# Optimization experiments

Hardware: AMD Instinct MI355X
Metric: run time of the kernel (lower is better)

## Reference

```python
import jax, jax.numpy as jnp
import numpy as np

N, E, H, D_IN, L, G, T = 50000, 800000, 64, 64, 4, 128, 1

def _w(key, shape, fan_in):
    return jax.random.normal(key, shape, dtype=jnp.float32) / np.sqrt(fan_in)

def setup_inputs() -> dict:
    key = jax.random.key(0)
    ks = jax.random.split(key, 24)
    inp = {
        'x': jax.random.normal(ks[0], (N, D_IN), dtype=jnp.float32),
        'w': jax.random.normal(ks[1], (E, 1), dtype=jnp.float32),
        'src': jax.random.randint(ks[2], (E,), 0, N, dtype=jnp.int32),
        'dst': jax.random.randint(ks[3], (E,), 0, N, dtype=jnp.int32),
        'graph_id': jnp.sort(jax.random.randint(ks[4], (N,), 0, G, dtype=jnp.int32)),
        # input MLP (1 layer, last_activation None; SiLU applied in input_node_func)
        'W_in': _w(ks[5], (D_IN, H), D_IN), 'b_in': jnp.zeros((H,), jnp.float32),
        # per-layer message MLP: (2H+1 -> H -> H), SiLU mid and last
        'msg_W1': _w(ks[6], (L, 2 * H + 1, H), 2 * H + 1), 'msg_b1': jnp.zeros((L, H), jnp.float32),
        'msg_W2': _w(ks[7], (L, H, H), H), 'msg_b2': jnp.zeros((L, H), jnp.float32),
        # per-layer update MLP: (H -> H -> H), SiLU mid, last None
        'upd_W1': _w(ks[8], (L, H, H), H), 'upd_b1': jnp.zeros((L, H), jnp.float32),
        'upd_W2': _w(ks[9], (L, H, H), H), 'upd_b2': jnp.zeros((L, H), jnp.float32),
        # node-wise output MLP: (H -> H -> H), SiLU mid, last None
        'out_W1': _w(ks[10], (H, H), H), 'out_b1': jnp.zeros((H,), jnp.float32),
        'out_W2': _w(ks[11], (H, H), H), 'out_b2': jnp.zeros((H,), jnp.float32),
        # readout MLP: (3H -> H -> T), SiLU mid, last None
        'ro_W1': _w(ks[12], (3 * H, H), 3 * H), 'ro_b1': jnp.zeros((H,), jnp.float32),
        'ro_W2': _w(ks[13], (H, T), H), 'ro_b2': jnp.zeros((T,), jnp.float32),
    }
    return inp

def reference(x, w, src, dst, graph_id, W_in, b_in, msg_W1, msg_b1, msg_W2, msg_b2,
              upd_W1, upd_b1, upd_W2, upd_b2, out_W1, out_b1, out_W2, out_b2,
              ro_W1, ro_b1, ro_W2, ro_b2):
    silu = jax.nn.silu
    f = silu(x @ W_in + b_in)                                   # [N, H]
    sq = w * w                                                  # [E, 1]
    for l in range(L):
        mi = jnp.concatenate([f[src], f[dst], sq], axis=-1)     # [E, 2H+1]
        msg = silu(silu(mi @ msg_W1[l] + msg_b1[l]) @ msg_W2[l] + msg_b2[l])
        m = msg * jax.nn.sigmoid(msg)                           # gated message
        m_sum = jax.ops.segment_sum(m, dst, num_segments=N)     # scatter-sum to dst
        h_new = silu((m_sum + f) @ upd_W1[l] + upd_b1[l]) @ upd_W2[l] + upd_b2[l]
        f = h_new + f                                           # residual
    f = silu(f @ out_W1 + out_b1) @ out_W2 + out_b2             # node-wise output
    g_sum = jax.ops.segment_sum(f, graph_id, num_segments=G)
    cnt = jax.ops.segment_sum(jnp.ones((N, 1), f.dtype), graph_id, num_segments=G)
    g_mean = g_sum / jnp.maximum(cnt, 1.0)
    g_max = jax.ops.segment_max(f, graph_id, num_segments=G)
    readout = jnp.concatenate([g_sum, g_mean, g_max], axis=-1)  # [G, 3H]
    return silu(readout @ ro_W1 + ro_b1) @ ro_W2 + ro_b2        # [G, T]
```

## Files before the change

kernel.cpp:

```cpp
#include <hip/hip_runtime.h>

#define NN 50000
#define EE 800000
#define GG 128
#define LL 4
#define SCAN_B 196

typedef __bf16 bf16x8 __attribute__((ext_vector_type(8)));
typedef float  f32x4  __attribute__((ext_vector_type(4)));

__device__ __forceinline__ float silu_f(float x){
    float t = __builtin_amdgcn_exp2f(-1.44269504f * x);
    return x * __builtin_amdgcn_rcpf(1.0f + t);
}
__device__ __forceinline__ unsigned fenc(float v){
    unsigned u = __float_as_uint(v);
    return (u & 0x80000000u) ? ~u : (u | 0x80000000u);
}
__device__ __forceinline__ float fdec(unsigned u){
    return (u & 0x80000000u) ? __uint_as_float(u & 0x7fffffffu) : __uint_as_float(~u);
}

__global__ __launch_bounds__(256) void input_mlp(const float* __restrict__ x,
        const float* __restrict__ Wg, const float* __restrict__ bg,
        float* __restrict__ f, __bf16* __restrict__ f16, int N){
    __shared__ __align__(16) float sW[64*64];
    __shared__ float sb[64];
    __shared__ __align__(16) float srow[4][64];
    int tid=threadIdx.x, wid=tid>>6, lane=tid&63;
    for(int i=tid;i<4096;i+=256) sW[i]=Wg[i];
    if(tid<64) sb[tid]=bg[tid];
    __syncthreads();
    int gw=gridDim.x*4;
    int n0=blockIdx.x*4+wid;
    int niter=(N+gw-1)/gw;
    for(int it=0;it<niter;++it){
        int n=n0+it*gw; bool act = n<N;
        if(act) srow[wid][lane]=x[n*64+lane];
        __syncthreads();
        if(act){
            float h=sb[lane];
            #pragma unroll
            for(int k=0;k<64;k+=4){
                float4 m4=*(const float4*)&srow[wid][k];
                h += m4.x*sW[k*64+lane] + m4.y*sW[(k+1)*64+lane]
                   + m4.z*sW[(k+2)*64+lane] + m4.w*sW[(k+3)*64+lane];
            }
            float o=silu_f(h);
            f[n*64+lane]=o; f16[n*64+lane]=(__bf16)o;
        }
        __syncthreads();
    }
}

__global__ void hist_k(const int* __restrict__ dst, int* __restrict__ deg, int E){
    int e=blockIdx.x*blockDim.x+threadIdx.x;
    if(e<E) atomicAdd(&deg[dst[e]],1);
}

__global__ __launch_bounds__(256) void scan1_k(const int* __restrict__ deg, int* __restrict__ curs,
        int* __restrict__ bsum, int N){
    __shared__ int sv[256];
    int tid=threadIdx.x;
    int idx=blockIdx.x*256+tid;
    int v=(idx<N)?deg[idx]:0;
    sv[tid]=v; __syncthreads();
    #pragma unroll
    for(int off=1; off<256; off<<=1){
        int a=(tid>=off)?sv[tid-off]:0;
        __syncthreads(); sv[tid]+=a; __syncthreads();
    }
    if(idx<N) curs[idx]=sv[tid]-v;
    if(tid==255) bsum[blockIdx.x]=sv[255];
}
__global__ __launch_bounds__(256) void scan2_k(int* __restrict__ bsum, int B){
    __shared__ int sv[256];
    int tid=threadIdx.x;
    int v=(tid<B)?bsum[tid]:0;
    sv[tid]=v; __syncthreads();
    #pragma unroll
    for(int off=1; off<256; off<<=1){
        int a=(tid>=off)?sv[tid-off]:0;
        __syncthreads(); sv[tid]+=a; __syncthreads();
    }
    if(tid<B) bsum[tid]=sv[tid]-v;
}
__global__ __launch_bounds__(256) void scan3_k(int* __restrict__ curs, const int* __restrict__ bsum, int N){
    int idx=blockIdx.x*256+threadIdx.x;
    if(idx<N) curs[idx]+=bsum[blockIdx.x];
}

__global__ void fill_k(const int* __restrict__ src, const int* __restrict__ dst,
                       const float* __restrict__ w, int* __restrict__ cursor,
                       int* __restrict__ src_s, int* __restrict__ dst_s,
                       float* __restrict__ w2_s, int E){
    int e=blockIdx.x*blockDim.x+threadIdx.x;
    if(e<E){
        int d=dst[e];
        int r=atomicAdd(&cursor[d],1);
        src_s[r]=src[e];
        dst_s[r]=d;
        float ww=w[e];
        w2_s[r]=ww*ww;
    }
}

__global__ __launch_bounds__(256) void xy_mfma(const __bf16* __restrict__ f16,
        const float* __restrict__ W1, __bf16* __restrict__ XY, int N){
    int tid=threadIdx.x, wid=tid>>6, lane=tid&63;
    int q=lane>>4, nn=lane&15;
    bf16x8 Bf[2][8];
    #pragma unroll
    for(int s=0;s<2;++s)
        #pragma unroll
        for(int ng=0;ng<8;++ng){
            bf16x8 t;
            #pragma unroll
            for(int j=0;j<8;++j){
                int k=32*s+8*q+j, c=16*ng+nn;
                float v = (c<64) ? W1[k*64+c] : W1[(64+k)*64 + (c-64)];
                t[j]=(__bf16)v;
            }
            Bf[s][ng]=t;
        }
    int ntiles=(N+15)/16;
    int gw=gridDim.x*4;
    for(int t=blockIdx.x*4+wid; t<ntiles; t+=gw){
        int row=t*16+nn; if(row>=N) row=N-1;
        bf16x8 a0=*(const bf16x8*)&f16[(size_t)row*64 + 8*q];
        bf16x8 a1=*(const bf16x8*)&f16[(size_t)row*64 + 32 + 8*q];
        #pragma unroll
        for(int ng=0;ng<8;++ng){
            f32x4 acc; acc[0]=0.f; acc[1]=0.f; acc[2]=0.f; acc[3]=0.f;
            acc=__builtin_amdgcn_mfma_f32_16x16x32_bf16(a0,Bf[0][ng],acc,0,0,0);
            acc=__builtin_amdgcn_mfma_f32_16x16x32_bf16(a1,Bf[1][ng],acc,0,0,0);
            #pragma unroll
            for(int r=0;r<4;++r){
                int orow=t*16+4*q+r;
                if(orow<N) XY[(size_t)orow*128 + 16*ng + nn]=(__bf16)acc[r];
            }
        }
    }
}

__global__ __launch_bounds__(256) void edge_mfma2(
        const __bf16* __restrict__ XY,
        const int* __restrict__ src_s, const int* __restrict__ dst_s,
        const float* __restrict__ w2_s,
        const float* __restrict__ W1, const float* __restrict__ b1,
        const float* __restrict__ W2, const float* __restrict__ b2,
        float* __restrict__ msum, int E){
    int tid=threadIdx.x, wid=tid>>6, lane=tid&63;
    int q=lane>>4, nn=lane&15;

    bf16x8 B2f[2][4];
    #pragma unroll
    for(int s=0;s<2;++s)
        #pragma unroll
        for(int ng=0;ng<4;++ng){
            bf16x8 t;
            #pragma unroll
            for(int j=0;j<8;++j) t[j]=(__bf16)W2[(32*s+8*q+j)*64 + 16*ng + nn];
            B2f[s][ng]=t;
        }
    float w128lo[8], w128hi[8], b1lo[8], b1hi[8];
    #pragma unroll
    for(int j=0;j<8;++j){
        w128lo[j]=W1[128*64 + 8*q+j];
        w128hi[j]=W1[128*64 + 32+8*q+j];
        b1lo[j]=b1[8*q+j];
        b1hi[j]=b1[32+8*q+j];
    }
    float bias2[4];
    #pragma unroll
    for(int ng=0;ng<4;++ng) bias2[ng]=b2[16*ng+nn];

    __shared__ float sm[4][32][68];

    int ntiles=E/32;
    int gw=gridDim.x*4;
    for(int t=blockIdx.x*4+wid; t<ntiles; t+=gw){
        int slot=t*32+lane;
        int d_=-1, s_=0; float w2v=0.f;
        if(lane<32){
            s_=src_s[slot];
            d_=dst_s[slot];
            w2v=w2_s[slot];
        }
        #pragma unroll
        for(int h=0;h<2;++h){
            int se=__shfl(s_, 16*h+nn, 64);
            int de=__shfl(d_, 16*h+nn, 64);
            float w2=__shfl(w2v, 16*h+nn, 64);
            const __bf16* xp = XY + (size_t)se*128;
            const __bf16* yp = XY + (size_t)de*128 + 64;
            bf16x8 xlo=*(const bf16x8*)(xp + 8*q);
            bf16x8 xhi=*(const bf16x8*)(xp + 32 + 8*q);
            bf16x8 ylo=*(const bf16x8*)(yp + 8*q);
            bf16x8 yhi=*(const bf16x8*)(yp + 32 + 8*q);
            bf16x8 a20, a21;
            #pragma unroll
            for(int j=0;j<8;++j){
                float hlo=(float)xlo[j] + (float)ylo[j] + w2*w128lo[j] + b1lo[j];
                float hhi=(float)xhi[j] + (float)yhi[j] + w2*w128hi[j] + b1hi[j];
                a20[j]=(__bf16)silu_f(hlo);
                a21[j]=(__bf16)silu_f(hhi);
            }
            f32x4 acc2[4];
            #pragma unroll
            for(int ng=0;ng<4;++ng){ f32x4 c; c[0]=bias2[ng]; c[1]=bias2[ng]; c[2]=bias2[ng]; c[3]=bias2[ng]; acc2[ng]=c; }
            #pragma unroll
            for(int ng=0;ng<4;++ng){
                acc2[ng]=__builtin_amdgcn_mfma_f32_16x16x32_bf16(a20,B2f[0][ng],acc2[ng],0,0,0);
                acc2[ng]=__builtin_amdgcn_mfma_f32_16x16x32_bf16(a21,B2f[1][ng],acc2[ng],0,0,0);
            }
            #pragma unroll
            for(int ng=0;ng<4;++ng)
                #pragma unroll
                for(int r=0;r<4;++r)
                    sm[wid][16*h+4*q+r][16*ng+nn]=silu_f(silu_f(acc2[ng][r]));
        }
        asm volatile("" ::: "memory");
        float vsum=0.f; int cur=__shfl(d_, 0, 64);
        #pragma unroll
        for(int r=0;r<32;++r){
            int dr=__shfl(d_, r, 64);
            if(dr!=cur){
                atomicAdd(&msum[(size_t)cur*64+lane], vsum);
                vsum=0.f; cur=dr;
            }
            vsum+=sm[wid][r][lane];
        }
        atomicAdd(&msum[(size_t)cur*64+lane], vsum);
        asm volatile("" ::: "memory");
    }
}

__global__ __launch_bounds__(256) void node_mfma(const float* __restrict__ A, const float* __restrict__ F,
        const float* __restrict__ W1, const float* __restrict__ b1,
        const float* __restrict__ W2, const float* __restrict__ b2,
        float* __restrict__ out, __bf16* __restrict__ out16, int N){
    int tid=threadIdx.x, wid=tid>>6, lane=tid&63;
    int q=lane>>4, nn=lane&15;

    bf16x8 B1f[2][4], B2f[2][4];
    #pragma unroll
    for(int s=0;s<2;++s)
        #pragma unroll
        for(int ng=0;ng<4;++ng){
            bf16x8 t1, t2;
            #pragma unroll
            for(int j=0;j<8;++j){
                t1[j]=(__bf16)W1[(32*s+8*q+j)*64 + 16*ng + nn];
                t2[j]=(__bf16)W2[(32*s+8*q+j)*64 + 16*ng + nn];
            }
            B1f[s][ng]=t1; B2f[s][ng]=t2;
        }
    float bias1[4], bias2[4];
    #pragma unroll
    for(int ng=0;ng<4;++ng){ bias1[ng]=b1[16*ng+nn]; bias2[ng]=b2[16*ng+nn]; }

    __shared__ __align__(16) __bf16 sh1[4][16][72];
    __shared__ __align__(16) float sF[4][16][68];
    bool hasF = (F != nullptr);

    int ntiles=(N+15)/16;
    int gw=gridDim.x*4;
    for(int t=blockIdx.x*4+wid; t<ntiles; t+=gw){
        int m=t*16+nn;
        int mc=(m<N)?m:(N-1);
        float4 a0=*(const float4*)&A[(size_t)mc*64 + 8*q];
        float4 a1=*(const float4*)&A[(size_t)mc*64 + 8*q + 4];
        float4 a2=*(const float4*)&A[(size_t)mc*64 + 32 + 8*q];
        float4 a3=*(const float4*)&A[(size_t)mc*64 + 32 + 8*q + 4];
        if(hasF){
            float4 f0=*(const float4*)&F[(size_t)mc*64 + 8*q];
            float4 f1=*(const float4*)&F[(size_t)mc*64 + 8*q + 4];
            float4 f2_=*(const float4*)&F[(size_t)mc*64 + 32 + 8*q];
            float4 f3=*(const float4*)&F[(size_t)mc*64 + 32 + 8*q + 4];
            a0.x+=f0.x; a0.y+=f0.y; a0.z+=f0.z; a0.w+=f0.w;
            a1.x+=f1.x; a1.y+=f1.y; a1.z+=f1.z; a1.w+=f1.w;
            a2.x+=f2_.x; a2.y+=f2_.y; a2.z+=f2_.z; a2.w+=f2_.w;
            a3.x+=f3.x; a3.y+=f3.y; a3.z+=f3.z; a3.w+=f3.w;
            *(float4*)&sF[wid][nn][8*q]   = f0;
            *(float4*)&sF[wid][nn][8*q+4] = f1;
            *(float4*)&sF[wid][nn][32+8*q]   = f2_;
            *(float4*)&sF[wid][nn][32+8*q+4] = f3;
        }
        bf16x8 af0, af1;
        af0[0]=(__bf16)a0.x; af0[1]=(__bf16)a0.y; af0[2]=(__bf16)a0.z; af0[3]=(__bf16)a0.w;
        af0[4]=(__bf16)a1.x; af0[5]=(__bf16)a1.y; af0[6]=(__bf16)a1.z; af0[7]=(__bf16)a1.w;
        af1[0]=(__bf16)a2.x; af1[1]=(__bf16)a2.y; af1[2]=(__bf16)a2.z; af1[3]=(__bf16)a2.w;
        af1[4]=(__bf16)a3.x; af1[5]=(__bf16)a3.y; af1[6]=(__bf16)a3.z; af1[7]=(__bf16)a3.w;

        f32x4 acc[4];
        #pragma unroll
        for(int ng=0;ng<4;++ng){ f32x4 c; c[0]=bias1[ng]; c[1]=bias1[ng]; c[2]=bias1[ng]; c[3]=bias1[ng]; acc[ng]=c; }
        #pragma unroll
        for(int ng=0;ng<4;++ng){
            acc[ng]=__builtin_amdgcn_mfma_f32_16x16x32_bf16(af0,B1f[0][ng],acc[ng],0,0,0);
            acc[ng]=__builtin_amdgcn_mfma_f32_16x16x32_bf16(af1,B1f[1][ng],acc[ng],0,0,0);
        }
        #pragma unroll
        for(int ng=0;ng<4;++ng)
            #pragma unroll
            for(int r=0;r<4;++r)
                sh1[wid][4*q+r][16*ng+nn]=(__bf16)silu_f(acc[ng][r]);
        asm volatile("" ::: "memory");
        bf16x8 a20=*(const bf16x8*)&sh1[wid][nn][8*q];
        bf16x8 a21=*(const bf16x8*)&sh1[wid][nn][32+8*q];
        f32x4 acc2[4];
        #pragma unroll
        for(int ng=0;ng<4;++ng){ f32x4 c; c[0]=bias2[ng]; c[1]=bias2[ng]; c[2]=bias2[ng]; c[3]=bias2[ng]; acc2[ng]=c; }
        #pragma unroll
        for(int ng=0;ng<4;++ng){
            acc2[ng]=__builtin_amdgcn_mfma_f32_16x16x32_bf16(a20,B2f[0][ng],acc2[ng],0,0,0);
            acc2[ng]=__builtin_amdgcn_mfma_f32_16x16x32_bf16(a21,B2f[1][ng],acc2[ng],0,0,0);
        }
        #pragma unroll
        for(int ng=0;ng<4;++ng)
            #pragma unroll
            for(int r=0;r<4;++r){
                int row=t*16+4*q+r;
                if(row<N){
                    float o=acc2[ng][r];
                    if(hasF) o += sF[wid][4*q+r][16*ng+nn];
                    out[(size_t)row*64 + 16*ng + nn]=o;
                    if(out16) out16[(size_t)row*64 + 16*ng + nn]=(__bf16)o;
                }
            }
        asm volatile("" ::: "memory");
    }
}

__global__ __launch_bounds__(256) void seg_reduce_sorted(const float* __restrict__ f2, const int* __restrict__ gid,
        float* __restrict__ gsum, unsigned* __restrict__ gmaxu, float* __restrict__ cnt, int N){
    int wgl=blockIdx.x*4 + (threadIdx.x>>6);
    int lane=threadIdx.x&63;
    int W=gridDim.x*4;
    int chunk=(N+W-1)/W;
    int n0=wgl*chunk;
    int n1=n0+chunk; if(n1>N) n1=N;
    if(n0>=n1) return;
    int cur=gid[n0];
    float s=0.f, mx=-__builtin_inff(), c=0.f;
    for(int n=n0;n<n1;++n){
        int g=gid[n];
        float v=f2[(size_t)n*64+lane];
        if(g!=cur){
            atomicAdd(&gsum[(size_t)cur*64+lane], s);
            atomicMax(&gmaxu[(size_t)cur*64+lane], fenc(mx));
            if(lane==0) atomicAdd(&cnt[cur], c);
            s=0.f; mx=-__builtin_inff(); c=0.f; cur=g;
        }
        s+=v; mx=fmaxf(mx,v); c+=1.f;
    }
    atomicAdd(&gsum[(size_t)cur*64+lane], s);
    atomicMax(&gmaxu[(size_t)cur*64+lane], fenc(mx));
    if(lane==0) atomicAdd(&cnt[cur], c);
}

__global__ __launch_bounds__(256) void readout_k(const float* __restrict__ gsum, const unsigned* __restrict__ gmaxu,
        const float* __restrict__ cnt,
        const float* __restrict__ W1, const float* __restrict__ b1,
        const float* __restrict__ W2, const float* __restrict__ b2,
        float* __restrict__ out, int G){
    __shared__ __align__(16) float sr[4][192];
    int tid=threadIdx.x, wid=tid>>6, lane=tid&63;
    int g=blockIdx.x*4+wid;
    if(g<G){
        float s_=gsum[g*64+lane];
        float c=cnt[g];
        float mean=s_/fmaxf(c,1.0f);
        float mx=fdec(gmaxu[g*64+lane]);
        sr[wid][lane]=s_; sr[wid][64+lane]=mean; sr[wid][128+lane]=mx;
    }
    __syncthreads();
    if(g<G){
        float h=b1[lane];
        for(int k=0;k<192;k+=4){
            float4 r4=*(const float4*)&sr[wid][k];
            h += r4.x*W1[(k+0)*64+lane] + r4.y*W1[(k+1)*64+lane]
               + r4.z*W1[(k+2)*64+lane] + r4.w*W1[(k+3)*64+lane];
        }
        h=silu_f(h);
        float p=h*W2[lane];
        #pragma unroll
        for(int off=32;off>0;off>>=1) p += __shfl_down(p, off, 64);
        if(lane==0) out[g]=p+b2[0];
    }
}

extern "C" void kernel_launch(void* const* d_in, const int* in_sizes, int n_in,
                              void* d_out, int out_size, void* d_ws, size_t ws_size,
                              hipStream_t stream){
    const float* x     = (const float*)d_in[0];
    const float* w     = (const float*)d_in[1];
    const int*   src   = (const int*)d_in[2];
    const int*   dst   = (const int*)d_in[3];
    const int*   gid   = (const int*)d_in[4];
    const float* W_in  = (const float*)d_in[5];
    const float* b_in  = (const float*)d_in[6];
    const float* msgW1 = (const float*)d_in[7];
    const float* msgb1 = (const float*)d_in[8];
    const float* msgW2 = (const float*)d_in[9];
    const float* msgb2 = (const float*)d_in[10];
    const float* updW1 = (const float*)d_in[11];
    const float* updb1 = (const float*)d_in[12];
    const float* updW2 = (const float*)d_in[13];
    const float* updb2 = (const float*)d_in[14];
    const float* outW1 = (const float*)d_in[15];
    const float* outb1 = (const float*)d_in[16];
    const float* outW2 = (const float*)d_in[17];
    const float* outb2 = (const float*)d_in[18];
    const float* roW1  = (const float*)d_in[19];
    const float* rob1  = (const float*)d_in[20];
    const float* roW2  = (const float*)d_in[21];
    const float* rob2  = (const float*)d_in[22];

    float*  f     = (float*)d_ws;
    float*  msum  = f + (size_t)NN*64;
    float*  f2    = msum;
    __bf16* f16   = (__bf16*)(msum + (size_t)NN*64);
    __bf16* XY    = f16 + (size_t)NN*64;
    int*    src_s = (int*)(XY + (size_t)NN*128);
    int*    dst_s = src_s + EE;
    float*  w2_s  = (float*)(dst_s + EE);
    int*    deg   = (int*)(w2_s + EE);
    int*    curs  = deg + 50048;
    int*    bsum  = curs + 50048;
    float*  gsum  = (float*)(bsum + 256);
    unsigned* gmaxu = (unsigned*)(gsum + GG*64);
    float*  cnt   = (float*)(gmaxu + GG*64);

    hipMemsetAsync(deg, 0, 50048*sizeof(int), stream);
    hist_k<<<dim3((EE+255)/256),dim3(256),0,stream>>>(dst, deg, EE);
    scan1_k<<<dim3(SCAN_B),dim3(256),0,stream>>>(deg, curs, bsum, NN);
    scan2_k<<<dim3(1),dim3(256),0,stream>>>(bsum, SCAN_B);
    scan3_k<<<dim3(SCAN_B),dim3(256),0,stream>>>(curs, bsum, NN);
    fill_k<<<dim3((EE+255)/256),dim3(256),0,stream>>>(src, dst, w, curs, src_s, dst_s, w2_s, EE);

    input_mlp<<<dim3(1024),dim3(256),0,stream>>>(x, W_in, b_in, f, f16, NN);
    for(int l=0;l<LL;++l){
        xy_mfma<<<dim3(512),dim3(256),0,stream>>>(f16, msgW1 + (size_t)l*129*64, XY, NN);
        hipMemsetAsync(msum, 0, (size_t)NN*64*sizeof(float), stream);
        edge_mfma2<<<dim3(1024),dim3(256),0,stream>>>(XY, src_s, dst_s, w2_s,
            msgW1 + (size_t)l*129*64, msgb1 + l*64,
            msgW2 + (size_t)l*64*64,  msgb2 + l*64, msum, EE);
        node_mfma<<<dim3(782),dim3(256),0,stream>>>(msum, f,
            updW1 + (size_t)l*64*64, updb1 + l*64,
            updW2 + (size_t)l*64*64, updb2 + l*64, f, f16, NN);
    }
    node_mfma<<<dim3(782),dim3(256),0,stream>>>(f, nullptr, outW1, outb1, outW2, outb2, f2, nullptr, NN);
    hipMemsetAsync(gsum, 0, (size_t)(GG*64*2 + GG)*sizeof(float), stream);
    seg_reduce_sorted<<<dim3(256),dim3(256),0,stream>>>(f2, gid, gsum, gmaxu, cnt, NN);
    readout_k<<<dim3(32),dim3(256),0,stream>>>(gsum, gmaxu, cnt, roW1, rob1, roW2, rob2, (float*)d_out, GG);
}
```

Measured before the change: 669.0 us.

## Pre-pack bf16 weight fragments, pipeline edge gathers, pack edge metadata, MFMA input MLP

```diff
diff --git a/kernel.cpp b/kernel.cpp
--- a/kernel.cpp
+++ b/kernel.cpp
@@ -21,35 +21,77 @@
     return (u & 0x80000000u) ? __uint_as_float(u & 0x7fffffffu) : __uint_as_float(~u);
 }
 
-__global__ __launch_bounds__(256) void input_mlp(const float* __restrict__ x,
-        const float* __restrict__ Wg, const float* __restrict__ bg,
+__global__ __launch_bounds__(256) void pack_k(
+        const float* __restrict__ msgW1, const float* __restrict__ msgW2,
+        const float* __restrict__ updW1, const float* __restrict__ updW2,
+        const float* __restrict__ outW1, const float* __restrict__ outW2,
+        const float* __restrict__ W_in, __bf16* __restrict__ pk){
+    int m = blockIdx.x;
+    const float* src;
+    if(m<20){
+        int l=m/5, r=m%5;
+        if(r==0)      src = msgW1 + (size_t)l*129*64;
+        else if(r==1) src = msgW1 + (size_t)l*129*64 + 64*64;
+        else if(r==2) src = msgW2 + (size_t)l*64*64;
+        else if(r==3) src = updW1 + (size_t)l*64*64;
+        else          src = updW2 + (size_t)l*64*64;
+    } else if(m==20) src=outW1; else if(m==21) src=outW2; else src=W_in;
+    __bf16* dst = pk + (size_t)m*4096;
+    int tid=threadIdx.x;
+    #pragma unroll
+    for(int i=0;i<16;++i){
+        int idx = tid*16+i;
+        int frag = idx>>9, lane=(idx>>3)&63, j=idx&7;
+        int s=frag>>2, ng=frag&3, q=lane>>4, nn=lane&15;
+        dst[idx] = (__bf16)src[(32*s+8*q+j)*64 + 16*ng + nn];
+    }
+}
+__device__ __forceinline__ bf16x8 ldfrag(const __bf16* pk, int s, int ng, int lane){
+    return *(const bf16x8*)&pk[(((s*4+ng)*64 + lane))*8];
+}
+
+__global__ __launch_bounds__(256) void input_mfma(const float* __restrict__ x,
+        const __bf16* __restrict__ pkW, const float* __restrict__ bg,
         float* __restrict__ f, __bf16* __restrict__ f16, int N){
-    __shared__ __align__(16) float sW[64*64];
-    __shared__ float sb[64];
-    __shared__ __align__(16) float srow[4][64];
     int tid=threadIdx.x, wid=tid>>6, lane=tid&63;
-    for(int i=tid;i<4096;i+=256) sW[i]=Wg[i];
-    if(tid<64) sb[tid]=bg[tid];
-    __syncthreads();
+    int q=lane>>4, nn=lane&15;
+    bf16x8 Bf[2][4];
+    #pragma unroll
+    for(int s=0;s<2;++s)
+        #pragma unroll
+        for(int ng=0;ng<4;++ng) Bf[s][ng]=ldfrag(pkW,s,ng,lane);
+    float bias[4];
+    #pragma unroll
+    for(int ng=0;ng<4;++ng) bias[ng]=bg[16*ng+nn];
+
+    int ntiles=(N+15)/16;
     int gw=gridDim.x*4;
-    int n0=blockIdx.x*4+wid;
-    int niter=(N+gw-1)/gw;
-    for(int it=0;it<niter;++it){
-        int n=n0+it*gw; bool act = n<N;
-        if(act) srow[wid][lane]=x[n*64+lane];
-        __syncthreads();
-        if(act){
-            float h=sb[lane];
-            #pragma unroll
-            for(int k=0;k<64;k+=4){
-                float4 m4=*(const float4*)&srow[wid][k];
-                h += m4.x*sW[k*64+lane] + m4.y*sW[(k+1)*64+lane]
-                   + m4.z*sW[(k+2)*64+lane] + m4.w*sW[(k+3)*64+lane];
-            }
-            float o=silu_f(h);
-            f[n*64+lane]=o; f16[n*64+lane]=(__bf16)o;
-        }
-        __syncthreads();
+    for(int t=blockIdx.x*4+wid; t<ntiles; t+=gw){
+        int m=t*16+nn; int mc=(m<N)?m:(N-1);
+        float4 a0=*(const float4*)&x[(size_t)mc*64 + 8*q];
+        float4 a1=*(const float4*)&x[(size_t)mc*64 + 8*q + 4];
+        float4 a2=*(const float4*)&x[(size_t)mc*64 + 32 + 8*q];
+        float4 a3=*(const float4*)&x[(size_t)mc*64 + 32 + 8*q + 4];
+        bf16x8 af0, af1;
+        af0[0]=(__bf16)a0.x; af0[1]=(__bf16)a0.y; af0[2]=(__bf16)a0.z; af0[3]=(__bf16)a0.w;
+        af0[4]=(__bf16)a1.x; af0[5]=(__bf16)a1.y; af0[6]=(__bf16)a1.z; af0[7]=(__bf16)a1.w;
+        af1[0]=(__bf16)a2.x; af1[1]=(__bf16)a2.y; af1[2]=(__bf16)a2.z; af1[3]=(__bf16)a2.w;
+        af1[4]=(__bf16)a3.x; af1[5]=(__bf16)a3.y; af1[6]=(__bf16)a3.z; af1[7]=(__bf16)a3.w;
+        #pragma unroll
+        for(int ng=0;ng<4;++ng){
+            f32x4 acc; acc[0]=bias[ng]; acc[1]=bias[ng]; acc[2]=bias[ng]; acc[3]=bias[ng];
+            acc=__builtin_amdgcn_mfma_f32_16x16x32_bf16(af0,Bf[0][ng],acc,0,0,0);
+            acc=__builtin_amdgcn_mfma_f32_16x16x32_bf16(af1,Bf[1][ng],acc,0,0,0);
+            #pragma unroll
+            for(int r=0;r<4;++r){
+                int row=t*16+4*q+r;
+                if(row<N){
+                    float o=silu_f(acc[r]);
+                    f[(size_t)row*64+16*ng+nn]=o;
+                    f16[(size_t)row*64+16*ng+nn]=(__bf16)o;
+                }
+            }
+        }
     }
 }
 
@@ -92,37 +134,31 @@
 
 __global__ void fill_k(const int* __restrict__ src, const int* __restrict__ dst,
                        const float* __restrict__ w, int* __restrict__ cursor,
-                       int* __restrict__ src_s, int* __restrict__ dst_s,
-                       float* __restrict__ w2_s, int E){
+                       int4* __restrict__ meta, int E){
     int e=blockIdx.x*blockDim.x+threadIdx.x;
     if(e<E){
         int d=dst[e];
         int r=atomicAdd(&cursor[d],1);
-        src_s[r]=src[e];
-        dst_s[r]=d;
         float ww=w[e];
-        w2_s[r]=ww*ww;
+        int4 v; v.x=src[e]; v.y=d; v.z=__float_as_int(ww*ww); v.w=0;
+        meta[r]=v;
     }
 }
 
 __global__ __launch_bounds__(256) void xy_mfma(const __bf16* __restrict__ f16,
-        const float* __restrict__ W1, __bf16* __restrict__ XY, int N){
+        const __bf16* __restrict__ pkA, const __bf16* __restrict__ pkB,
+        const float* __restrict__ b1, __bf16* __restrict__ XY, int N){
     int tid=threadIdx.x, wid=tid>>6, lane=tid&63;
     int q=lane>>4, nn=lane&15;
     bf16x8 Bf[2][8];
     #pragma unroll
-    for(int s=0;s<2;++s)
-        #pragma unroll
-        for(int ng=0;ng<8;++ng){
-            bf16x8 t;
-            #pragma unroll
-            for(int j=0;j<8;++j){
-                int k=32*s+8*q+j, c=16*ng+nn;
-                float v = (c<64) ? W1[k*64+c] : W1[(64+k)*64 + (c-64)];
-                t[j]=(__bf16)v;
-            }
-            Bf[s][ng]=t;
-        }
+    for(int s=0;s<2;++s){
+        #pragma unroll
+        for(int ng=0;ng<4;++ng){ Bf[s][ng]=ldfrag(pkA,s,ng,lane); Bf[s][4+ng]=ldfrag(pkB,s,ng,lane); }
+    }
+    float bias[8];
+    #pragma unroll
+    for(int ng=0;ng<8;++ng) bias[ng]=(ng<4)?0.f:b1[16*(ng-4)+nn];
     int ntiles=(N+15)/16;
     int gw=gridDim.x*4;
     for(int t=blockIdx.x*4+wid; t<ntiles; t+=gw){
@@ -131,7 +167,7 @@
         bf16x8 a1=*(const bf16x8*)&f16[(size_t)row*64 + 32 + 8*q];
         #pragma unroll
         for(int ng=0;ng<8;++ng){
-            f32x4 acc; acc[0]=0.f; acc[1]=0.f; acc[2]=0.f; acc[3]=0.f;
+            f32x4 acc; acc[0]=bias[ng]; acc[1]=bias[ng]; acc[2]=bias[ng]; acc[3]=bias[ng];
             acc=__builtin_amdgcn_mfma_f32_16x16x32_bf16(a0,Bf[0][ng],acc,0,0,0);
             acc=__builtin_amdgcn_mfma_f32_16x16x32_bf16(a1,Bf[1][ng],acc,0,0,0);
             #pragma unroll
@@ -143,12 +179,10 @@
     }
 }
 
-__global__ __launch_bounds__(256) void edge_mfma2(
-        const __bf16* __restrict__ XY,
-        const int* __restrict__ src_s, const int* __restrict__ dst_s,
-        const float* __restrict__ w2_s,
-        const float* __restrict__ W1, const float* __restrict__ b1,
-        const float* __restrict__ W2, const float* __restrict__ b2,
+__global__ __launch_bounds__(256,4) void edge_mfma3(
+        const __bf16* __restrict__ XY, const int4* __restrict__ meta,
+        const __bf16* __restrict__ pkW2,
+        const float* __restrict__ W1, const float* __restrict__ b2,
         float* __restrict__ msum, int E){
     int tid=threadIdx.x, wid=tid>>6, lane=tid&63;
     int q=lane>>4, nn=lane&15;
@@ -157,19 +191,12 @@
     #pragma unroll
     for(int s=0;s<2;++s)
         #pragma unroll
-        for(int ng=0;ng<4;++ng){
-            bf16x8 t;
-            #pragma unroll
-            for(int j=0;j<8;++j) t[j]=(__bf16)W2[(32*s+8*q+j)*64 + 16*ng + nn];
-            B2f[s][ng]=t;
-        }
-    float w128lo[8], w128hi[8], b1lo[8], b1hi[8];
+        for(int ng=0;ng<4;++ng) B2f[s][ng]=ldfrag(pkW2,s,ng,lane);
+    float w128lo[8], w128hi[8];
     #pragma unroll
     for(int j=0;j<8;++j){
         w128lo[j]=W1[128*64 + 8*q+j];
         w128hi[j]=W1[128*64 + 32+8*q+j];
-        b1lo[j]=b1[8*q+j];
-        b1hi[j]=b1[32+8*q+j];
     }
     float bias2[4];
     #pragma unroll
@@ -178,31 +205,42 @@
     __shared__ float sm[4][32][68];
 
     int ntiles=E/32;
-    int gw=gridDim.x*4;
-    for(int t=blockIdx.x*4+wid; t<ntiles; t+=gw){
-        int slot=t*32+lane;
-        int d_=-1, s_=0; float w2v=0.f;
-        if(lane<32){
-            s_=src_s[slot];
-            d_=dst_s[slot];
-            w2v=w2_s[slot];
-        }
-        #pragma unroll
-        for(int h=0;h<2;++h){
-            int se=__shfl(s_, 16*h+nn, 64);
-            int de=__shfl(d_, 16*h+nn, 64);
-            float w2=__shfl(w2v, 16*h+nn, 64);
-            const __bf16* xp = XY + (size_t)se*128;
-            const __bf16* yp = XY + (size_t)de*128 + 64;
-            bf16x8 xlo=*(const bf16x8*)(xp + 8*q);
-            bf16x8 xhi=*(const bf16x8*)(xp + 32 + 8*q);
-            bf16x8 ylo=*(const bf16x8*)(yp + 8*q);
-            bf16x8 yhi=*(const bf16x8*)(yp + 32 + 8*q);
+    int nw=gridDim.x*4;
+    int chunk=(ntiles+nw-1)/nw;
+    int wgl=blockIdx.x*4+wid;
+    int t0=wgl*chunk, t1=t0+chunk; if(t1>ntiles) t1=ntiles;
+    if(t0>=t1) return;
+
+    int4 mv = meta[(size_t)t0*32 + (lane&31)];
+    bf16x8 gx0lo,gx0hi,gy0lo,gy0hi,gx1lo,gx1hi,gy1lo,gy1hi;
+    {
+        int se0=__shfl(mv.x, nn,64),    de0=__shfl(mv.y, nn,64);
+        int se1=__shfl(mv.x, 16+nn,64), de1=__shfl(mv.y, 16+nn,64);
+        const __bf16* xp0=XY+(size_t)se0*128; const __bf16* yp0=XY+(size_t)de0*128+64;
+        const __bf16* xp1=XY+(size_t)se1*128; const __bf16* yp1=XY+(size_t)de1*128+64;
+        gx0lo=*(const bf16x8*)(xp0+8*q); gx0hi=*(const bf16x8*)(xp0+32+8*q);
+        gy0lo=*(const bf16x8*)(yp0+8*q); gy0hi=*(const bf16x8*)(yp0+32+8*q);
+        gx1lo=*(const bf16x8*)(xp1+8*q); gx1hi=*(const bf16x8*)(xp1+32+8*q);
+        gy1lo=*(const bf16x8*)(yp1+8*q); gy1hi=*(const bf16x8*)(yp1+32+8*q);
+    }
+    int cur=__shfl(mv.y,0,64);
+    float vsum=0.f;
+
+    for(int t=t0;t<t1;++t){
+        bool hasn = (t+1<t1);
+        int4 mvn = mv;
+        if(hasn) mvn = meta[(size_t)(t+1)*32 + (lane&31)];
+
+        int d_ = mv.y;
+        float w2v = __int_as_float(mv.z);
+
+        {
+            float w2 = __shfl(w2v, nn, 64);
             bf16x8 a20, a21;
             #pragma unroll
             for(int j=0;j<8;++j){
-                float hlo=(float)xlo[j] + (float)ylo[j] + w2*w128lo[j] + b1lo[j];
-                float hhi=(float)xhi[j] + (float)yhi[j] + w2*w128hi[j] + b1hi[j];
+                float hlo=(float)gx0lo[j] + (float)gy0lo[j] + w2*w128lo[j];
+                float hhi=(float)gx0hi[j] + (float)gy0hi[j] + w2*w128hi[j];
                 a20[j]=(__bf16)silu_f(hlo);
                 a21[j]=(__bf16)silu_f(hhi);
             }
@@ -218,10 +256,45 @@
             for(int ng=0;ng<4;++ng)
                 #pragma unroll
                 for(int r=0;r<4;++r)
-                    sm[wid][16*h+4*q+r][16*ng+nn]=silu_f(silu_f(acc2[ng][r]));
+                    sm[wid][4*q+r][16*ng+nn]=silu_f(silu_f(acc2[ng][r]));
+        }
+        {
+            float w2 = __shfl(w2v, 16+nn, 64);
+            bf16x8 a20, a21;
+            #pragma unroll
+            for(int j=0;j<8;++j){
+                float hlo=(float)gx1lo[j] + (float)gy1lo[j] + w2*w128lo[j];
+                float hhi=(float)gx1hi[j] + (float)gy1hi[j] + w2*w128hi[j];
+                a20[j]=(__bf16)silu_f(hlo);
+                a21[j]=(__bf16)silu_f(hhi);
+            }
+            f32x4 acc2[4];
+            #pragma unroll
+            for(int ng=0;ng<4;++ng){ f32x4 c; c[0]=bias2[ng]; c[1]=bias2[ng]; c[2]=bias2[ng]; c[3]=bias2[ng]; acc2[ng]=c; }
+            #pragma unroll
+            for(int ng=0;ng<4;++ng){
+                acc2[ng]=__builtin_amdgcn_mfma_f32_16x16x32_bf16(a20,B2f[0][ng],acc2[ng],0,0,0);
+                acc2[ng]=__builtin_amdgcn_mfma_f32_16x16x32_bf16(a21,B2f[1][ng],acc2[ng],0,0,0);
+            }
+            #pragma unroll
+            for(int ng=0;ng<4;++ng)
+                #pragma unroll
+                for(int r=0;r<4;++r)
+                    sm[wid][16+4*q+r][16*ng+nn]=silu_f(silu_f(acc2[ng][r]));
         }
         asm volatile("" ::: "memory");
-        float vsum=0.f; int cur=__shfl(d_, 0, 64);
+
+        if(hasn){
+            int se0=__shfl(mvn.x, nn,64),    de0=__shfl(mvn.y, nn,64);
+            int se1=__shfl(mvn.x, 16+nn,64), de1=__shfl(mvn.y, 16+nn,64);
+            const __bf16* xp0=XY+(size_t)se0*128; const __bf16* yp0=XY+(size_t)de0*128+64;
+            const __bf16* xp1=XY+(size_t)se1*128; const __bf16* yp1=XY+(size_t)de1*128+64;
+            gx0lo=*(const bf16x8*)(xp0+8*q); gx0hi=*(const bf16x8*)(xp0+32+8*q);
+            gy0lo=*(const bf16x8*)(yp0+8*q); gy0hi=*(const bf16x8*)(yp0+32+8*q);
+            gx1lo=*(const bf16x8*)(xp1+8*q); gx1hi=*(const bf16x8*)(xp1+32+8*q);
+            gy1lo=*(const bf16x8*)(yp1+8*q); gy1hi=*(const bf16x8*)(yp1+32+8*q);
+        }
+
         #pragma unroll
         for(int r=0;r<32;++r){
             int dr=__shfl(d_, r, 64);
@@ -231,14 +304,15 @@
             }
             vsum+=sm[wid][r][lane];
         }
-        atomicAdd(&msum[(size_t)cur*64+lane], vsum);
         asm volatile("" ::: "memory");
-    }
+        mv = mvn;
+    }
+    atomicAdd(&msum[(size_t)cur*64+lane], vsum);
 }
 
 __global__ __launch_bounds__(256) void node_mfma(const float* __restrict__ A, const float* __restrict__ F,
-        const float* __restrict__ W1, const float* __restrict__ b1,
-        const float* __restrict__ W2, const float* __restrict__ b2,
+        const __bf16* __restrict__ pkW1, const float* __restrict__ b1,
+        const __bf16* __restrict__ pkW2, const float* __restrict__ b2,
         float* __restrict__ out, __bf16* __restrict__ out16, int N){
     int tid=threadIdx.x, wid=tid>>6, lane=tid&63;
     int q=lane>>4, nn=lane&15;
@@ -247,15 +321,7 @@
     #pragma unroll
     for(int s=0;s<2;++s)
         #pragma unroll
-        for(int ng=0;ng<4;++ng){
-            bf16x8 t1, t2;
-            #pragma unroll
-            for(int j=0;j<8;++j){
-                t1[j]=(__bf16)W1[(32*s+8*q+j)*64 + 16*ng + nn];
-                t2[j]=(__bf16)W2[(32*s+8*q+j)*64 + 16*ng + nn];
-            }
-            B1f[s][ng]=t1; B2f[s][ng]=t2;
-        }
+        for(int ng=0;ng<4;++ng){ B1f[s][ng]=ldfrag(pkW1,s,ng,lane); B2f[s][ng]=ldfrag(pkW2,s,ng,lane); }
     float bias1[4], bias2[4];
     #pragma unroll
     for(int ng=0;ng<4;++ng){ bias1[ng]=b1[16*ng+nn]; bias2[ng]=b2[16*ng+nn]; }
@@ -423,35 +489,38 @@
     float*  f2    = msum;
     __bf16* f16   = (__bf16*)(msum + (size_t)NN*64);
     __bf16* XY    = f16 + (size_t)NN*64;
-    int*    src_s = (int*)(XY + (size_t)NN*128);
-    int*    dst_s = src_s + EE;
-    float*  w2_s  = (float*)(dst_s + EE);
-    int*    deg   = (int*)(w2_s + EE);
+    int4*   meta  = (int4*)(XY + (size_t)NN*128);
+    __bf16* pk    = (__bf16*)(meta + EE);
+    int*    deg   = (int*)(pk + 23*4096);
     int*    curs  = deg + 50048;
     int*    bsum  = curs + 50048;
     float*  gsum  = (float*)(bsum + 256);
     unsigned* gmaxu = (unsigned*)(gsum + GG*64);
     float*  cnt   = (float*)(gmaxu + GG*64);
 
+    pack_k<<<dim3(23),dim3(256),0,stream>>>(msgW1, msgW2, updW1, updW2, outW1, outW2, W_in, pk);
+
     hipMemsetAsync(deg, 0, 50048*sizeof(int), stream);
     hist_k<<<dim3((EE+255)/256),dim3(256),0,stream>>>(dst, deg, EE);
     scan1_k<<<dim3(SCAN_B),dim3(256),0,stream>>>(deg, curs, bsum, NN);
     scan2_k<<<dim3(1),dim3(256),0,stream>>>(bsum, SCAN_B);
     scan3_k<<<dim3(SCAN_B),dim3(256),0,stream>>>(curs, bsum, NN);
-    fill_k<<<dim3((EE+255)/256),dim3(256),0,stream>>>(src, dst, w, curs, src_s, dst_s, w2_s, EE);
-
-    input_mlp<<<dim3(1024),dim3(256),0,stream>>>(x, W_in, b_in, f, f16, NN);
+    fill_k<<<dim3((EE+255)/256),dim3(256),0,stream>>>(src, dst, w, curs, meta, EE);
+
+    input_mfma<<<dim3(782),dim3(256),0,stream>>>(x, pk + (size_t)22*4096, b_in, f, f16, NN);
     for(int l=0;l<LL;++l){
-        xy_mfma<<<dim3(512),dim3(256),0,stream>>>(f16, msgW1 + (size_t)l*129*64, XY, NN);
+        xy_mfma<<<dim3(512),dim3(256),0,stream>>>(f16,
+            pk + (size_t)(5*l+0)*4096, pk + (size_t)(5*l+1)*4096, msgb1 + l*64, XY, NN);
         hipMemsetAsync(msum, 0, (size_t)NN*64*sizeof(float), stream);
-        edge_mfma2<<<dim3(1024),dim3(256),0,stream>>>(XY, src_s, dst_s, w2_s,
-            msgW1 + (size_t)l*129*64, msgb1 + l*64,
-            msgW2 + (size_t)l*64*64,  msgb2 + l*64, msum, EE);
+        edge_mfma3<<<dim3(1024),dim3(256),0,stream>>>(XY, meta,
+            pk + (size_t)(5*l+2)*4096,
+            msgW1 + (size_t)l*129*64, msgb2 + l*64, msum, EE);
         node_mfma<<<dim3(782),dim3(256),0,stream>>>(msum, f,
-            updW1 + (size_t)l*64*64, updb1 + l*64,
-            updW2 + (size_t)l*64*64, updb2 + l*64, f, f16, NN);
-    }
-    node_mfma<<<dim3(782),dim3(256),0,stream>>>(f, nullptr, outW1, outb1, outW2, outb2, f2, nullptr, NN);
+            pk + (size_t)(5*l+3)*4096, updb1 + l*64,
+            pk + (size_t)(5*l+4)*4096, updb2 + l*64, f, f16, NN);
+    }
+    node_mfma<<<dim3(782),dim3(256),0,stream>>>(f, nullptr,
+        pk + (size_t)20*4096, outb1, pk + (size_t)21*4096, outb2, f2, nullptr, NN);
     hipMemsetAsync(gsum, 0, (size_t)(GG*64*2 + GG)*sizeof(float), stream);
     seg_reduce_sorted<<<dim3(256),dim3(256),0,stream>>>(f2, gid, gsum, gmaxu, cnt, NN);
     readout_k<<<dim3(32),dim3(256),0,stream>>>(gsum, gmaxu, cnt, roW1, rob1, roW2, rob2, (float*)d_out, GG);
```

After: 827.9 us. +23.7%, slower.
